# Kernel optimization log

Hardware: AMD Instinct MI355X
Metric: run time of the kernel (lower is better)

## Reference

```python
import jax, jax.numpy as jnp
import numpy as np

N_NODES = 100000
N_EDGES = 800000
D = 128
N_GRAPHS = 512


def _graph_conv(h, src, dst, norm_src, norm_dst, W, b):
    # DGL GraphConv, norm='both': h' = relu(D_in^{-1/2} * sum_{(u->v)} (D_out^{-1/2} h_u) W + b)
    m = (h * norm_src[:, None])[src]                      # [E, d] gather
    agg = jax.ops.segment_sum(m, dst, num_segments=N_NODES)  # [N, d] scatter-add
    return jax.nn.relu(agg * norm_dst[:, None] @ W + b)


def setup_inputs() -> dict:
    key = jax.random.key(0)
    ks = jax.random.split(key, 10)
    src = jax.random.randint(ks[0], (N_EDGES,), 0, N_NODES)
    dst = jax.random.randint(ks[1], (N_EDGES,), 0, N_NODES)
    graph_ids = jnp.sort(jax.random.randint(ks[2], (N_ODES := N_NODES,), 0, N_GRAPHS))
    features = jax.random.normal(ks[3], (N_NODES, D), dtype=jnp.float32)
    s = 1.0 / np.sqrt(D)
    w1 = jax.random.uniform(ks[4], (D, D), jnp.float32, -s, s)
    b1 = jnp.zeros((D,), jnp.float32)
    w2 = jax.random.uniform(ks[5], (D, D), jnp.float32, -s, s)
    b2 = jnp.zeros((D,), jnp.float32)
    wg = jax.random.uniform(ks[6], (D, 1), jnp.float32, -s, s)
    bg = jnp.zeros((1,), jnp.float32)
    return {"src": src, "dst": dst, "graph_ids": graph_ids, "features": features,
            "w1": w1, "b1": b1, "w2": w2, "b2": b2, "wg": wg, "bg": bg}


def reference(src, dst, graph_ids, features, w1, b1, w2, b2, wg, bg):
    ones = jnp.ones((N_EDGES,), jnp.float32)
    deg_out = jax.ops.segment_sum(ones, src, num_segments=N_NODES)
    deg_in = jax.ops.segment_sum(ones, dst, num_segments=N_NODES)
    norm_src = jax.lax.rsqrt(jnp.maximum(deg_out, 1.0))
    norm_dst = jax.lax.rsqrt(jnp.maximum(deg_in, 1.0))

    h = _graph_conv(features, src, dst, norm_src, norm_dst, w1, b1)
    # dropout is identity in eval mode
    h = _graph_conv(h, src, dst, norm_src, norm_dst, w2, b2)

    # weighted graph aggregation: sigmoid gate per node, per-graph weighted sum
    gate = jax.nn.sigmoid(h @ wg + bg)                    # [N, 1]
    wh = jax.ops.segment_sum(gate * h, graph_ids, num_segments=N_GRAPHS)  # [G, d]
    return wh, h
```

## Files before the change

kernel.cpp:

```cpp
#include <hip/hip_runtime.h>

#define D 128
#define G_GRAPHS 512
#define CCHUNK 4
#define NSLICE 128
#define BINMAX 25088

typedef _Float16 f16;
typedef _Float16 f16x2 __attribute__((ext_vector_type(2)));
typedef _Float16 f16x4 __attribute__((ext_vector_type(4)));
typedef _Float16 f16x8 __attribute__((ext_vector_type(8)));
typedef float f32x2 __attribute__((ext_vector_type(2)));
typedef float f32x4 __attribute__((ext_vector_type(4)));
typedef unsigned short u16;
typedef unsigned char u8;

#define SCAN_CHUNK 2048

__device__ __forceinline__ f16x8 dq8(uint2 w) {
    f32x2 p0 = __builtin_amdgcn_cvt_pk_f32_fp8((int)w.x, false);
    f32x2 p1 = __builtin_amdgcn_cvt_pk_f32_fp8((int)w.x, true);
    f32x2 p2 = __builtin_amdgcn_cvt_pk_f32_fp8((int)w.y, false);
    f32x2 p3 = __builtin_amdgcn_cvt_pk_f32_fp8((int)w.y, true);
    f16x8 r;
    r[0] = (f16)p0.x; r[1] = (f16)p0.y; r[2] = (f16)p1.x; r[3] = (f16)p1.y;
    r[4] = (f16)p2.x; r[5] = (f16)p2.y; r[6] = (f16)p3.x; r[7] = (f16)p3.y;
    return r;
}

__global__ __launch_bounds__(256) void hist_kernel(const int* __restrict__ src, const int* __restrict__ dst,
                                                   u8* __restrict__ pho, u8* __restrict__ phi,
                                                   u8* __restrict__ rank,
                                                   int E, int N, int slice_len, int binsz) {
    __shared__ unsigned hp[(BINMAX + 3) / 4];
    int c = blockIdx.x, role = blockIdx.y, s = blockIdx.z;
    int c0 = c * binsz;
    int lim = min(binsz, N - c0);
    int nw = (lim + 3) >> 2;
    for (int i = threadIdx.x; i < nw; i += 256) hp[i] = 0;
    __syncthreads();
    const int* arr = role ? dst : src;
    int e1 = min(E, (s + 1) * slice_len);
    if (role) {
        for (int e = s * slice_len + (int)threadIdx.x; e < e1; e += 256) {
            unsigned v = (unsigned)(arr[e] - c0);
            if (v < (unsigned)lim) {
                int sh = (v & 3) * 8;
                unsigned old = atomicAdd(&hp[v >> 2], 1u << sh);
                rank[e] = (u8)((old >> sh) & 0xffu);
            }
        }
    } else {
        for (int e = s * slice_len + (int)threadIdx.x; e < e1; e += 256) {
            unsigned v = (unsigned)(arr[e] - c0);
            if (v < (unsigned)lim)
                atomicAdd(&hp[v >> 2], 1u << ((v & 3) * 8));
        }
    }
    __syncthreads();
    u8* outp = (role ? phi : pho) + (size_t)s * N + c0;
    int nw4 = lim >> 2;
    unsigned* o32 = (unsigned*)outp;
    for (int i = threadIdx.x; i < nw4; i += 256) o32[i] = hp[i];
    for (int i = nw4 * 4 + (int)threadIdx.x; i < lim; i += 256)
        outp[i] = (u8)((hp[i >> 2] >> ((i & 3) * 8)) & 0xffu);
}

__global__ __launch_bounds__(256) void merge_prescale_kernel(const u8* __restrict__ pho, u8* __restrict__ phi,
                                                             const float* __restrict__ feat,
                                                             float* __restrict__ norm_src, float* __restrict__ norm_dst,
                                                             int* __restrict__ deg_in_total,
                                                             unsigned* __restrict__ X1,
                                                             const int* __restrict__ gid, int* __restrict__ gstart,
                                                             int* __restrict__ ticket,
                                                             int mb, int N, int G) {
    if (blockIdx.x == 0 && threadIdx.x == 0) *ticket = 0;
    if ((int)blockIdx.x >= mb) {
        int n = ((int)blockIdx.x - mb) * 256 + (int)threadIdx.x;
        if (n >= N) return;
        int g = gid[n];
        if (n == 0) {
            for (int x = 0; x <= g; ++x) gstart[x] = 0;
        } else {
            int pg = gid[n - 1];
            for (int x = pg + 1; x <= g; ++x) gstart[x] = n;
        }
        if (n == N - 1) {
            for (int x = g + 1; x <= G; ++x) gstart[x] = N;
        }
        return;
    }
    __shared__ int sumo[4][64];
    __shared__ int sumi[4][64];
    __shared__ float ns_l[64];
    int nl = threadIdx.x & 63;
    int sg = threadIdx.x >> 6;
    int nbase = blockIdx.x * 64;
    int n = nbase + nl;
    int ph_vals[32];
    int po = 0, pp = 0;
    if (n < N) {
        #pragma unroll 8
        for (int j = 0; j < 32; ++j) {
            int s = sg * 32 + j;
            po += pho[(size_t)s * N + n];
            int v = phi[(size_t)s * N + n];
            ph_vals[j] = v;
            pp += v;
        }
    }
    sumo[sg][nl] = po;
    sumi[sg][nl] = pp;
    __syncthreads();
    if (n < N) {
        int base_i = 0;
        #pragma unroll
        for (int g = 0; g < 4; ++g) base_i += (g < sg) ? sumi[g][nl] : 0;
        int run = base_i;
        #pragma unroll 8
        for (int j = 0; j < 32; ++j) {
            int s = sg * 32 + j;
            phi[(size_t)s * N + n] = (u8)run;
            run += ph_vals[j];
        }
        if (sg == 0) {
            int tot_o = sumo[0][nl] + sumo[1][nl] + sumo[2][nl] + sumo[3][nl];
            int tot_i = sumi[0][nl] + sumi[1][nl] + sumi[2][nl] + sumi[3][nl];
            float nsv = rsqrtf(fmaxf((float)tot_o, 1.0f));
            norm_src[n] = nsv;
            ns_l[nl] = nsv;
            deg_in_total[n] = tot_i;
            norm_dst[n] = rsqrtf(fmaxf((float)tot_i, 1.0f));
        }
    }
    __syncthreads();
    int cnt = (min(64, N - nbase)) * 32;
    const float4* f4 = (const float4*)feat + (size_t)nbase * 32;
    unsigned* o4 = X1 + (size_t)nbase * 32;
    for (int k = threadIdx.x; k < cnt; k += 256) {
        float4 v = f4[k];
        float s = ns_l[k >> 5];
        int pk = __builtin_amdgcn_cvt_pk_fp8_f32(v.x * s, v.y * s, 0, false);
        pk = __builtin_amdgcn_cvt_pk_fp8_f32(v.z * s, v.w * s, pk, true);
        o4[k] = (unsigned)pk;
    }
}

__global__ __launch_bounds__(256) void scan1_kernel(const int* __restrict__ deg,
                                                    int* __restrict__ partial,
                                                    int* __restrict__ blocksums,
                                                    int* __restrict__ ticket, int n, int nb) {
    __shared__ int wsum[4];
    __shared__ int lastflag;
    int lane = threadIdx.x & 63, wid = threadIdx.x >> 6;
    int base = blockIdx.x * SCAN_CHUNK + (int)threadIdx.x * 8;
    int v[8]; int tsum = 0;
    #pragma unroll
    for (int i = 0; i < 8; ++i) { v[i] = (base + i < n) ? deg[base + i] : 0; tsum += v[i]; }
    int s = tsum;
    #pragma unroll
    for (int off = 1; off < 64; off <<= 1) {
        int t = __shfl_up(s, off);
        if (lane >= off) s += t;
    }
    if (lane == 63) wsum[wid] = s;
    __syncthreads();
    int woff = 0;
    for (int w = 0; w < wid; ++w) woff += wsum[w];
    int run = woff + s - tsum;
    #pragma unroll
    for (int i = 0; i < 8; ++i) {
        if (base + i < n) partial[base + i] = run;
        run += v[i];
        if (base + i == n - 1) partial[n] = run;
    }
    if (threadIdx.x == 255) {
        __hip_atomic_store(&blocksums[blockIdx.x], woff + s, __ATOMIC_RELEASE, __HIP_MEMORY_SCOPE_AGENT);
        int old = __hip_atomic_fetch_add(ticket, 1, __ATOMIC_ACQ_REL, __HIP_MEMORY_SCOPE_AGENT);
        lastflag = (old == (int)gridDim.x - 1);
    }
    __syncthreads();
    if (lastflag && threadIdx.x < 64) {
        int l = threadIdx.x;
        int carry = 0;
        for (int b0 = 0; b0 < nb; b0 += 64) {
            int i = b0 + l;
            int bv = (i < nb) ? __hip_atomic_load(&blocksums[i], __ATOMIC_ACQUIRE, __HIP_MEMORY_SCOPE_AGENT) : 0;
            int ss = bv;
            #pragma unroll
            for (int off = 1; off < 64; off <<= 1) {
                int t = __shfl_up(ss, off);
                if (l >= off) ss += t;
            }
            if (i < nb) blocksums[i] = carry + ss - bv;
            carry += __shfl(ss, 63);
        }
    }
}

__global__ __launch_bounds__(256) void fill_kernel(const int* __restrict__ src, const int* __restrict__ dst,
                                                   const int* __restrict__ partial, const int* __restrict__ bs,
                                                   const u8* __restrict__ phi, const u8* __restrict__ rank,
                                                   int* __restrict__ csr_src,
                                                   int E, int N, int slice_len) {
    int s = blockIdx.y;
    int e = s * slice_len + blockIdx.x * 256 + threadIdx.x;
    int e1 = min(E, (s + 1) * slice_len);
    if (e >= e1) return;
    int d = dst[e];
    int p = partial[d] + bs[d >> 11] + (int)phi[(size_t)s * N + d] + (int)rank[e];
    csr_src[p] = src[e];
}

#define GATHER_BLOCKS 2048
__global__ __launch_bounds__(256) void gather_kernel(const unsigned* __restrict__ x,
                                                     const float* __restrict__ norm_dst,
                                                     const int* __restrict__ partial, const int* __restrict__ bs,
                                                     const int* __restrict__ csr_src,
                                                     unsigned* __restrict__ A, int N) {
    int wid0 = blockIdx.x * 4 + ((int)threadIdx.x >> 6);
    int lane = threadIdx.x & 63;
    int g = lane >> 4;
    int l = lane & 15;
    for (int node0 = wid0; node0 < N; node0 += GATHER_BLOCKS * 4) {
        int node = __builtin_amdgcn_readfirstlane(node0);
        int beg = partial[node] + bs[node >> 11];
        int end = partial[node + 1] + bs[(node + 1) >> 11];
        float acc0[8] = {0.f}, acc1[8] = {0.f};
        int e = beg;
        for (; e + 8 <= end; e += 8) {
            int sa = csr_src[e + g];
            int sb = csr_src[e + 4 + g];
            uint2 wa = *(const uint2*)(x + (size_t)sa * 32 + l * 2);
            uint2 wb = *(const uint2*)(x + (size_t)sb * 32 + l * 2);
            f32x2 p0 = __builtin_amdgcn_cvt_pk_f32_fp8((int)wa.x, false);
            f32x2 p1 = __builtin_amdgcn_cvt_pk_f32_fp8((int)wa.x, true);
            f32x2 p2 = __builtin_amdgcn_cvt_pk_f32_fp8((int)wa.y, false);
            f32x2 p3 = __builtin_amdgcn_cvt_pk_f32_fp8((int)wa.y, true);
            acc0[0] += p0.x; acc0[1] += p0.y; acc0[2] += p1.x; acc0[3] += p1.y;
            acc0[4] += p2.x; acc0[5] += p2.y; acc0[6] += p3.x; acc0[7] += p3.y;
            f32x2 q0 = __builtin_amdgcn_cvt_pk_f32_fp8((int)wb.x, false);
            f32x2 q1 = __builtin_amdgcn_cvt_pk_f32_fp8((int)wb.x, true);
            f32x2 q2 = __builtin_amdgcn_cvt_pk_f32_fp8((int)wb.y, false);
            f32x2 q3 = __builtin_amdgcn_cvt_pk_f32_fp8((int)wb.y, true);
            acc1[0] += q0.x; acc1[1] += q0.y; acc1[2] += q1.x; acc1[3] += q1.y;
            acc1[4] += q2.x; acc1[5] += q2.y; acc1[6] += q3.x; acc1[7] += q3.y;
        }
        if (e + 4 <= end) {
            int sa = csr_src[e + g];
            uint2 wa = *(const uint2*)(x + (size_t)sa * 32 + l * 2);
            f32x2 p0 = __builtin_amdgcn_cvt_pk_f32_fp8((int)wa.x, false);
            f32x2 p1 = __builtin_amdgcn_cvt_pk_f32_fp8((int)wa.x, true);
            f32x2 p2 = __builtin_amdgcn_cvt_pk_f32_fp8((int)wa.y, false);
            f32x2 p3 = __builtin_amdgcn_cvt_pk_f32_fp8((int)wa.y, true);
            acc0[0] += p0.x; acc0[1] += p0.y; acc0[2] += p1.x; acc0[3] += p1.y;
            acc0[4] += p2.x; acc0[5] += p2.y; acc0[6] += p3.x; acc0[7] += p3.y;
            e += 4;
        }
        int rem = end - e;
        if (g < rem) {
            int sa = csr_src[e + g];
            uint2 wa = *(const uint2*)(x + (size_t)sa * 32 + l * 2);
            f32x2 p0 = __builtin_amdgcn_cvt_pk_f32_fp8((int)wa.x, false);
            f32x2 p1 = __builtin_amdgcn_cvt_pk_f32_fp8((int)wa.x, true);
            f32x2 p2 = __builtin_amdgcn_cvt_pk_f32_fp8((int)wa.y, false);
            f32x2 p3 = __builtin_amdgcn_cvt_pk_f32_fp8((int)wa.y, true);
            acc1[0] += p0.x; acc1[1] += p0.y; acc1[2] += p1.x; acc1[3] += p1.y;
            acc1[4] += p2.x; acc1[5] += p2.y; acc1[6] += p3.x; acc1[7] += p3.y;
        }
        float nd = norm_dst[node];
        float vv[8];
        #pragma unroll
        for (int j = 0; j < 8; ++j) {
            float v = acc0[j] + acc1[j];
            v += __shfl_xor(v, 16);
            v += __shfl_xor(v, 32);
            vv[j] = v * nd;
        }
        if (g == 0) {
            int pk0 = __builtin_amdgcn_cvt_pk_fp8_f32(vv[0], vv[1], 0, false);
            pk0 = __builtin_amdgcn_cvt_pk_fp8_f32(vv[2], vv[3], pk0, true);
            int pk1 = __builtin_amdgcn_cvt_pk_fp8_f32(vv[4], vv[5], 0, false);
            pk1 = __builtin_amdgcn_cvt_pk_fp8_f32(vv[6], vv[7], pk1, true);
            uint2 o; o.x = (unsigned)pk0; o.y = (unsigned)pk1;
            *(uint2*)(A + (size_t)node * 32 + l * 2) = o;
        }
    }
}

template <typename OutT, bool FP8OUT, bool SCALE, bool GATE>
__global__ __launch_bounds__(256) void gemm_kernel(const unsigned* __restrict__ A8,
                                                   const float* __restrict__ Wg,
                                                   const float* __restrict__ bias,
                                                   const float* __restrict__ rowscale,
                                                   const float* __restrict__ wgv,
                                                   const float* __restrict__ bgv,
                                                   float* __restrict__ gate_out,
                                                   OutT* __restrict__ out, int M) {
    __shared__ f16 Wf[4 * 8 * 64 * 8];
    for (int i = threadIdx.x; i < 2048; i += 256) {
        int kg = i >> 7, j = i & 127;
        int k0 = kg * 8;
        f16x8 tmp;
        #pragma unroll
        for (int b = 0; b < 8; ++b) tmp[b] = (f16)Wg[(k0 + b) * D + j];
        int t = k0 >> 5, c = j >> 4;
        int l = ((k0 & 31) >> 3) * 16 + (j & 15);
        *(f16x8*)&Wf[((t * 8 + c) * 64 + l) * 8] = tmp;
    }
    __syncthreads();
    int wave = threadIdx.x >> 6, lane = threadIdx.x & 63;
    const uint2* A2 = (const uint2*)A8;

    for (int row0 = (blockIdx.x * 4 + wave) * 16; row0 < M; row0 += gridDim.x * 64) {
        int arow = row0 + (lane & 15);
        f16x8 a[4];
        #pragma unroll
        for (int t = 0; t < 4; ++t)
            a[t] = dq8(A2[(size_t)arow * 16 + t * 4 + (lane >> 4)]);

        float ns[4];
        if (SCALE) {
            #pragma unroll
            for (int r = 0; r < 4; ++r) ns[r] = rowscale[row0 + (lane >> 4) * 4 + r];
        }
        float dotr[4] = {0.f, 0.f, 0.f, 0.f};

        #pragma unroll
        for (int c = 0; c < 8; ++c) {
            f32x4 acc = {0.f, 0.f, 0.f, 0.f};
            #pragma unroll
            for (int t = 0; t < 4; ++t) {
                f16x8 bf = *(const f16x8*)&Wf[((t * 8 + c) * 64 + lane) * 8];
                acc = __builtin_amdgcn_mfma_f32_16x16x32_f16(a[t], bf, acc, 0, 0, 0);
            }
            int col = c * 16 + (lane & 15);
            float bj = bias[col];
            float wgc = GATE ? wgv[col] : 0.f;
            #pragma unroll
            for (int r = 0; r < 4; ++r) {
                int row = row0 + (lane >> 4) * 4 + r;
                float v = fmaxf(acc[r] + bj, 0.f);
                if (SCALE) v *= ns[r];
                if (FP8OUT) {
                    int pk = __builtin_amdgcn_cvt_pk_fp8_f32(v, v, 0, false);
                    ((u8*)out)[(size_t)row * D + col] = (u8)(pk & 0xff);
                } else {
                    out[(size_t)row * D + col] = (OutT)v;
                }
                if (GATE) dotr[r] += v * wgc;
            }
        }
        if (GATE) {
            float bg0 = bgv[0];
            #pragma unroll
            for (int r = 0; r < 4; ++r) {
                float d = dotr[r];
                d += __shfl_xor(d, 1); d += __shfl_xor(d, 2);
                d += __shfl_xor(d, 4); d += __shfl_xor(d, 8);
                if ((lane & 15) == 0)
                    gate_out[row0 + (lane >> 4) * 4 + r] = 1.0f / (1.0f + __expf(-(d + bg0)));
            }
        }
    }
}

__global__ __launch_bounds__(256) void gagg_kernel(const float* __restrict__ h,
                                                   const float* __restrict__ gate,
                                                   const int* __restrict__ gstart,
                                                   float* __restrict__ wh) {
    __shared__ float part[4][D];
    int g = blockIdx.x;
    int wave = threadIdx.x >> 6, lane = threadIdx.x & 63;
    int beg = gstart[g], end = gstart[g + 1];
    float2 acc = {0.f, 0.f};
    for (int n = beg + wave; n < end; n += 4) {
        float gv = gate[n];
        float2 hv = ((const float2*)(h + n * D))[lane];
        acc.x += gv * hv.x;
        acc.y += gv * hv.y;
    }
    part[wave][lane * 2]     = acc.x;
    part[wave][lane * 2 + 1] = acc.y;
    __syncthreads();
    if (wave == 0) {
        float sx = 0.f, sy = 0.f;
        #pragma unroll
        for (int w = 0; w < 4; ++w) { sx += part[w][lane * 2]; sy += part[w][lane * 2 + 1]; }
        float2 o = {sx, sy};
        ((float2*)(wh + g * D))[lane] = o;
    }
}

extern "C" void kernel_launch(void* const* d_in, const int* in_sizes, int n_in,
                              void* d_out, int out_size, void* d_ws, size_t ws_size,
                              hipStream_t stream) {
    const int*   src  = (const int*)d_in[0];
    const int*   dst  = (const int*)d_in[1];
    const int*   gid  = (const int*)d_in[2];
    const float* feat = (const float*)d_in[3];
    const float* w1   = (const float*)d_in[4];
    const float* b1   = (const float*)d_in[5];
    const float* w2   = (const float*)d_in[6];
    const float* b2   = (const float*)d_in[7];
    const float* wg   = (const float*)d_in[8];
    const float* bg   = (const float*)d_in[9];
    int E = in_sizes[0];
    int N = in_sizes[2];
    const int G = G_GRAPHS;

    int binsz     = (N + CCHUNK - 1) / CCHUNK;
    int slice_len = (E + NSLICE - 1) / NSLICE;
    int bps       = (slice_len + 255) / 256;

    char* ws = (char*)d_ws;
    size_t off = 0;
    auto carve = [&](size_t bytes) { void* p = ws + off; off = (off + bytes + 255) & ~(size_t)255; return p; };
    u8*       pho       = (u8*)      carve((size_t)NSLICE * N);
    u8*       phi       = (u8*)      carve((size_t)NSLICE * N);
    u8*       rank      = (u8*)      carve((size_t)E);
    float*    norm_src  = (float*)   carve((size_t)N * 4);
    float*    norm_dst  = (float*)   carve((size_t)N * 4);
    int*      deg_in_t  = (int*)     carve((size_t)N * 4);
    int*      partial   = (int*)     carve((size_t)(N + 1) * 4);
    int*      blocksums = (int*)     carve((size_t)64 * 4);
    int*      ticket    = (int*)     carve((size_t)256);
    int*      csr_src   = (int*)     carve((size_t)E * 4);
    unsigned* X1        = (unsigned*)carve((size_t)N * D);
    unsigned* X2        = (unsigned*)carve((size_t)N * D);
    unsigned* A         = (unsigned*)carve((size_t)N * D);
    float*    gate      = (float*)   carve((size_t)N * 4);
    int*      gstart    = (int*)     carve((size_t)(G + 1) * 4);

    float* wh_out = (float*)d_out;
    float* h_out  = (float*)d_out + (size_t)G * D;

    int nb = (N + SCAN_CHUNK - 1) / SCAN_CHUNK;
    int mb = (N + 63) / 64;
    int gb = (N + 255) / 256;

    dim3 hgrid(CCHUNK, 2, NSLICE);
    hist_kernel<<<hgrid, 256, 0, stream>>>(src, dst, pho, phi, rank, E, N, slice_len, binsz);
    merge_prescale_kernel<<<mb + gb, 256, 0, stream>>>(pho, phi, feat, norm_src, norm_dst,
                                                       deg_in_t, X1, gid, gstart, ticket, mb, N, G);

    scan1_kernel<<<nb, 256, 0, stream>>>(deg_in_t, partial, blocksums, ticket, N, nb);
    dim3 fgrid(bps, NSLICE);
    fill_kernel<<<fgrid, 256, 0, stream>>>(src, dst, partial, blocksums, phi, rank, csr_src, E, N, slice_len);

    gather_kernel<<<GATHER_BLOCKS, 256, 0, stream>>>(X1, norm_dst, partial, blocksums, csr_src, A, N);
    gemm_kernel<u8, true, true, false><<<256, 256, 0, stream>>>(A, w1, b1, norm_src, nullptr, nullptr, nullptr,
                                                                (u8*)X2, N);
    gather_kernel<<<GATHER_BLOCKS, 256, 0, stream>>>(X2, norm_dst, partial, blocksums, csr_src, A, N);
    gemm_kernel<float, false, false, true><<<256, 256, 0, stream>>>(A, w2, b2, nullptr, wg, bg, gate, h_out, N);

    gagg_kernel<<<G, 256, 0, stream>>>(h_out, gate, gstart, wh_out);
}
```

Baseline: 183.9 us.

## Halve histogram slices, widen hist blocks, and use 16-byte loads in gather

The histogram pass now uses 64 slices instead of 128 with 512-thread blocks, which halves the per-slice histogram arrays that the merge kernel reads and rewrites. The merge loop is adjusted to 16 slices per subgroup. The gather kernel now has 8 lanes per edge each loading 16 bytes, so 8 edges are processed per step, down from 16 lanes with 8-byte loads. This cuts the loop to one load per lane per iteration at the cost of an extra shuffle stage. Fewer slices means more edges per slice, which raises the risk that a u8 per-slice count or rank overflows for high-degree nodes.

```diff
diff --git a/kernel.cpp b/kernel.cpp
--- a/kernel.cpp
+++ b/kernel.cpp
@@ -3,7 +3,7 @@
 #define D 128
 #define G_GRAPHS 512
 #define CCHUNK 4
-#define NSLICE 128
+#define NSLICE 64
 #define BINMAX 25088
 
 typedef _Float16 f16;
@@ -28,7 +28,7 @@
     return r;
 }
 
-__global__ __launch_bounds__(256) void hist_kernel(const int* __restrict__ src, const int* __restrict__ dst,
+__global__ __launch_bounds__(512) void hist_kernel(const int* __restrict__ src, const int* __restrict__ dst,
                                                    u8* __restrict__ pho, u8* __restrict__ phi,
                                                    u8* __restrict__ rank,
                                                    int E, int N, int slice_len, int binsz) {
@@ -37,12 +37,12 @@
     int c0 = c * binsz;
     int lim = min(binsz, N - c0);
     int nw = (lim + 3) >> 2;
-    for (int i = threadIdx.x; i < nw; i += 256) hp[i] = 0;
+    for (int i = threadIdx.x; i < nw; i += 512) hp[i] = 0;
     __syncthreads();
     const int* arr = role ? dst : src;
     int e1 = min(E, (s + 1) * slice_len);
     if (role) {
-        for (int e = s * slice_len + (int)threadIdx.x; e < e1; e += 256) {
+        for (int e = s * slice_len + (int)threadIdx.x; e < e1; e += 512) {
             unsigned v = (unsigned)(arr[e] - c0);
             if (v < (unsigned)lim) {
                 int sh = (v & 3) * 8;
@@ -51,7 +51,7 @@
             }
         }
     } else {
-        for (int e = s * slice_len + (int)threadIdx.x; e < e1; e += 256) {
+        for (int e = s * slice_len + (int)threadIdx.x; e < e1; e += 512) {
             unsigned v = (unsigned)(arr[e] - c0);
             if (v < (unsigned)lim)
                 atomicAdd(&hp[v >> 2], 1u << ((v & 3) * 8));
@@ -61,8 +61,8 @@
     u8* outp = (role ? phi : pho) + (size_t)s * N + c0;
     int nw4 = lim >> 2;
     unsigned* o32 = (unsigned*)outp;
-    for (int i = threadIdx.x; i < nw4; i += 256) o32[i] = hp[i];
-    for (int i = nw4 * 4 + (int)threadIdx.x; i < lim; i += 256)
+    for (int i = threadIdx.x; i < nw4; i += 512) o32[i] = hp[i];
+    for (int i = nw4 * 4 + (int)threadIdx.x; i < lim; i += 512)
         outp[i] = (u8)((hp[i >> 2] >> ((i & 3) * 8)) & 0xffu);
 }
 
@@ -97,12 +97,12 @@
     int sg = threadIdx.x >> 6;
     int nbase = blockIdx.x * 64;
     int n = nbase + nl;
-    int ph_vals[32];
+    int ph_vals[16];
     int po = 0, pp = 0;
     if (n < N) {
-        #pragma unroll 8
-        for (int j = 0; j < 32; ++j) {
-            int s = sg * 32 + j;
+        #pragma unroll
+        for (int j = 0; j < 16; ++j) {
+            int s = sg * 16 + j;
             po += pho[(size_t)s * N + n];
             int v = phi[(size_t)s * N + n];
             ph_vals[j] = v;
@@ -117,9 +117,9 @@
         #pragma unroll
         for (int g = 0; g < 4; ++g) base_i += (g < sg) ? sumi[g][nl] : 0;
         int run = base_i;
-        #pragma unroll 8
-        for (int j = 0; j < 32; ++j) {
-            int s = sg * 32 + j;
+        #pragma unroll
+        for (int j = 0; j < 16; ++j) {
+            int s = sg * 16 + j;
             phi[(size_t)s * N + n] = (u8)run;
             run += ph_vals[j];
         }
@@ -220,59 +220,47 @@
                                                      unsigned* __restrict__ A, int N) {
     int wid0 = blockIdx.x * 4 + ((int)threadIdx.x >> 6);
     int lane = threadIdx.x & 63;
-    int g = lane >> 4;
-    int l = lane & 15;
+    int g = lane >> 3;
+    int l = lane & 7;
     for (int node0 = wid0; node0 < N; node0 += GATHER_BLOCKS * 4) {
         int node = __builtin_amdgcn_readfirstlane(node0);
         int beg = partial[node] + bs[node >> 11];
         int end = partial[node + 1] + bs[(node + 1) >> 11];
-        float acc0[8] = {0.f}, acc1[8] = {0.f};
+        float acc[16] = {0.f};
         int e = beg;
         for (; e + 8 <= end; e += 8) {
             int sa = csr_src[e + g];
-            int sb = csr_src[e + 4 + g];
-            uint2 wa = *(const uint2*)(x + (size_t)sa * 32 + l * 2);
-            uint2 wb = *(const uint2*)(x + (size_t)sb * 32 + l * 2);
-            f32x2 p0 = __builtin_amdgcn_cvt_pk_f32_fp8((int)wa.x, false);
-            f32x2 p1 = __builtin_amdgcn_cvt_pk_f32_fp8((int)wa.x, true);
-            f32x2 p2 = __builtin_amdgcn_cvt_pk_f32_fp8((int)wa.y, false);
-            f32x2 p3 = __builtin_amdgcn_cvt_pk_f32_fp8((int)wa.y, true);
-            acc0[0] += p0.x; acc0[1] += p0.y; acc0[2] += p1.x; acc0[3] += p1.y;
-            acc0[4] += p2.x; acc0[5] += p2.y; acc0[6] += p3.x; acc0[7] += p3.y;
-            f32x2 q0 = __builtin_amdgcn_cvt_pk_f32_fp8((int)wb.x, false);
-            f32x2 q1 = __builtin_amdgcn_cvt_pk_f32_fp8((int)wb.x, true);
-            f32x2 q2 = __builtin_amdgcn_cvt_pk_f32_fp8((int)wb.y, false);
-            f32x2 q3 = __builtin_amdgcn_cvt_pk_f32_fp8((int)wb.y, true);
-            acc1[0] += q0.x; acc1[1] += q0.y; acc1[2] += q1.x; acc1[3] += q1.y;
-            acc1[4] += q2.x; acc1[5] += q2.y; acc1[6] += q3.x; acc1[7] += q3.y;
-        }
-        if (e + 4 <= end) {
-            int sa = csr_src[e + g];
-            uint2 wa = *(const uint2*)(x + (size_t)sa * 32 + l * 2);
-            f32x2 p0 = __builtin_amdgcn_cvt_pk_f32_fp8((int)wa.x, false);
-            f32x2 p1 = __builtin_amdgcn_cvt_pk_f32_fp8((int)wa.x, true);
-            f32x2 p2 = __builtin_amdgcn_cvt_pk_f32_fp8((int)wa.y, false);
-            f32x2 p3 = __builtin_amdgcn_cvt_pk_f32_fp8((int)wa.y, true);
-            acc0[0] += p0.x; acc0[1] += p0.y; acc0[2] += p1.x; acc0[3] += p1.y;
-            acc0[4] += p2.x; acc0[5] += p2.y; acc0[6] += p3.x; acc0[7] += p3.y;
-            e += 4;
+            uint4 wa = *(const uint4*)(x + (size_t)sa * 32 + l * 4);
+            f32x2 p;
+            p = __builtin_amdgcn_cvt_pk_f32_fp8((int)wa.x, false); acc[0] += p.x;  acc[1] += p.y;
+            p = __builtin_amdgcn_cvt_pk_f32_fp8((int)wa.x, true);  acc[2] += p.x;  acc[3] += p.y;
+            p = __builtin_amdgcn_cvt_pk_f32_fp8((int)wa.y, false); acc[4] += p.x;  acc[5] += p.y;
+            p = __builtin_amdgcn_cvt_pk_f32_fp8((int)wa.y, true);  acc[6] += p.x;  acc[7] += p.y;
+            p = __builtin_amdgcn_cvt_pk_f32_fp8((int)wa.z, false); acc[8] += p.x;  acc[9] += p.y;
+            p = __builtin_amdgcn_cvt_pk_f32_fp8((int)wa.z, true);  acc[10] += p.x; acc[11] += p.y;
+            p = __builtin_amdgcn_cvt_pk_f32_fp8((int)wa.w, false); acc[12] += p.x; acc[13] += p.y;
+            p = __builtin_amdgcn_cvt_pk_f32_fp8((int)wa.w, true);  acc[14] += p.x; acc[15] += p.y;
         }
         int rem = end - e;
         if (g < rem) {
             int sa = csr_src[e + g];
-            uint2 wa = *(const uint2*)(x + (size_t)sa * 32 + l * 2);
-            f32x2 p0 = __builtin_amdgcn_cvt_pk_f32_fp8((int)wa.x, false);
-            f32x2 p1 = __builtin_amdgcn_cvt_pk_f32_fp8((int)wa.x, true);
-            f32x2 p2 = __builtin_amdgcn_cvt_pk_f32_fp8((int)wa.y, false);
-            f32x2 p3 = __builtin_amdgcn_cvt_pk_f32_fp8((int)wa.y, true);
-            acc1[0] += p0.x; acc1[1] += p0.y; acc1[2] += p1.x; acc1[3] += p1.y;
-            acc1[4] += p2.x; acc1[5] += p2.y; acc1[6] += p3.x; acc1[7] += p3.y;
+            uint4 wa = *(const uint4*)(x + (size_t)sa * 32 + l * 4);
+            f32x2 p;
+            p = __builtin_amdgcn_cvt_pk_f32_fp8((int)wa.x, false); acc[0] += p.x;  acc[1] += p.y;
+            p = __builtin_amdgcn_cvt_pk_f32_fp8((int)wa.x, true);  acc[2] += p.x;  acc[3] += p.y;
+            p = __builtin_amdgcn_cvt_pk_f32_fp8((int)wa.y, false); acc[4] += p.x;  acc[5] += p.y;
+            p = __builtin_amdgcn_cvt_pk_f32_fp8((int)wa.y, true);  acc[6] += p.x;  acc[7] += p.y;
+            p = __builtin_amdgcn_cvt_pk_f32_fp8((int)wa.z, false); acc[8] += p.x;  acc[9] += p.y;
+            p = __builtin_amdgcn_cvt_pk_f32_fp8((int)wa.z, true);  acc[10] += p.x; acc[11] += p.y;
+            p = __builtin_amdgcn_cvt_pk_f32_fp8((int)wa.w, false); acc[12] += p.x; acc[13] += p.y;
+            p = __builtin_amdgcn_cvt_pk_f32_fp8((int)wa.w, true);  acc[14] += p.x; acc[15] += p.y;
         }
         float nd = norm_dst[node];
-        float vv[8];
-        #pragma unroll
-        for (int j = 0; j < 8; ++j) {
-            float v = acc0[j] + acc1[j];
+        float vv[16];
+        #pragma unroll
+        for (int j = 0; j < 16; ++j) {
+            float v = acc[j];
+            v += __shfl_xor(v, 8);
             v += __shfl_xor(v, 16);
             v += __shfl_xor(v, 32);
             vv[j] = v * nd;
@@ -282,8 +270,12 @@
             pk0 = __builtin_amdgcn_cvt_pk_fp8_f32(vv[2], vv[3], pk0, true);
             int pk1 = __builtin_amdgcn_cvt_pk_fp8_f32(vv[4], vv[5], 0, false);
             pk1 = __builtin_amdgcn_cvt_pk_fp8_f32(vv[6], vv[7], pk1, true);
-            uint2 o; o.x = (unsigned)pk0; o.y = (unsigned)pk1;
-            *(uint2*)(A + (size_t)node * 32 + l * 2) = o;
+            int pk2 = __builtin_amdgcn_cvt_pk_fp8_f32(vv[8], vv[9], 0, false);
+            pk2 = __builtin_amdgcn_cvt_pk_fp8_f32(vv[10], vv[11], pk2, true);
+            int pk3 = __builtin_amdgcn_cvt_pk_fp8_f32(vv[12], vv[13], 0, false);
+            pk3 = __builtin_amdgcn_cvt_pk_fp8_f32(vv[14], vv[15], pk3, true);
+            uint4 o; o.x = (unsigned)pk0; o.y = (unsigned)pk1; o.z = (unsigned)pk2; o.w = (unsigned)pk3;
+            *(uint4*)(A + (size_t)node * 32 + l * 4) = o;
         }
     }
 }
@@ -440,7 +432,7 @@
     int gb = (N + 255) / 256;
 
     dim3 hgrid(CCHUNK, 2, NSLICE);
-    hist_kernel<<<hgrid, 256, 0, stream>>>(src, dst, pho, phi, rank, E, N, slice_len, binsz);
+    hist_kernel<<<hgrid, 512, 0, stream>>>(src, dst, pho, phi, rank, E, N, slice_len, binsz);
     merge_prescale_kernel<<<mb + gb, 256, 0, stream>>>(pho, phi, feat, norm_src, norm_dst,
                                                        deg_in_t, X1, gid, gstart, ticket, mb, N, G);
 
```

Result: slower. 231.7 us (+26.0%).
